# Performance work log

Hardware: AMD Instinct MI355X
Metric: run time of the kernel (lower is better)

The kernel has to match this reference:

```python
import jax, jax.numpy as jnp
import numpy as np

NODE_DIM = 128
INSTR_DIM = 128
HIDDEN_DIM = 256
N_NODES = 50000
N_EDGES = 800000
N_GRAPHS = 64


def setup_inputs() -> dict:
    key = jax.random.key(0)
    k_instr, k_x, k_ei, k_b, k_w1, k_b1, k_w2, k_b2 = jax.random.split(key, 8)
    instr = jax.random.normal(k_instr, (N_GRAPHS, INSTR_DIM), dtype=jnp.float32)
    x = jax.random.normal(k_x, (N_NODES, NODE_DIM), dtype=jnp.float32)
    edge_index = jax.random.randint(k_ei, (2, N_EDGES), 0, N_NODES, dtype=jnp.int64)
    batch = jnp.sort(jax.random.randint(k_b, (N_NODES,), 0, N_GRAPHS, dtype=jnp.int64))
    in_dim = 2 * NODE_DIM + INSTR_DIM  # 384
    lim1 = 1.0 / np.sqrt(in_dim)
    lim2 = 1.0 / np.sqrt(HIDDEN_DIM)
    W1 = jax.random.uniform(k_w1, (in_dim, HIDDEN_DIM), jnp.float32, -lim1, lim1)
    b1 = jax.random.uniform(k_b1, (HIDDEN_DIM,), jnp.float32, -lim1, lim1)
    W2 = jax.random.uniform(k_w2, (HIDDEN_DIM, 1), jnp.float32, -lim2, lim2)
    b2 = jax.random.uniform(k_b2, (1,), jnp.float32, -lim2, lim2)
    return {"instr": instr, "x": x, "edge_index": edge_index, "batch": batch,
            "W1": W1, "b1": b1, "W2": W2, "b2": b2}


def reference(instr, x, edge_index, batch, W1, b1, W2, b2):
    src, dst = edge_index[0], edge_index[1]
    u = instr[batch[src]]                       # [E, Di] gather via batch[src]
    h = jnp.concatenate([x[src], x[dst], u], axis=-1)  # [E, 2D+Di]
    h = jax.nn.silu(h @ W1 + b1)                # [E, H] (dropout p=0 -> identity)
    logits = (h @ W2 + b2).squeeze(-1)          # [E]
    return logits
```

## Files before the change

kernel.cpp:

```cpp
#include <hip/hip_runtime.h>
#include <hip/hip_bf16.h>
#include <stdint.h>

#define E_EDGES   800000
#define N_NODES_C 50000
#define NG        64
#define DD        128
#define HH        256
#define KDIM      384

typedef __bf16 bf16x8 __attribute__((ext_vector_type(8)));
typedef __bf16 bf16x4 __attribute__((ext_vector_type(4)));
typedef float  f32x4  __attribute__((ext_vector_type(4)));
typedef uint32_t u32x4 __attribute__((ext_vector_type(4)));

__device__ __forceinline__ void gld16(const void* g, void* l) {
  __builtin_amdgcn_global_load_lds(
      (__attribute__((address_space(1))) void*)g,
      (__attribute__((address_space(3))) void*)l, 16, 0, 0);
}

__device__ __forceinline__ float bf_hi(uint32_t u) { return __uint_as_float(u & 0xffff0000u); }
__device__ __forceinline__ float bf_lo(uint32_t u) { return __uint_as_float(u << 16); }

#define PREP_CVT_BLKS 6250
#define PREP_W1_BLKS  256
#define PREP_R2_BLKS  64

__global__ void k_prep(const float* __restrict__ x, const float* __restrict__ w1,
                       const float* __restrict__ instr, const float* __restrict__ b1,
                       __bf16* __restrict__ xbf, __bf16* __restrict__ w1pt,
                       float* __restrict__ r2) {
  __shared__ float ins[DD];
  const int bid = blockIdx.x;
  const int tid = threadIdx.x;
  if (bid < PREP_CVT_BLKS) {
    int i = bid * 256 + tid;
    float4 v = ((const float4*)x)[i];
    bf16x4 b;
    b[0] = (__bf16)v.x; b[1] = (__bf16)v.y; b[2] = (__bf16)v.z; b[3] = (__bf16)v.w;
    ((bf16x4*)xbf)[i] = b;
  } else if (bid < PREP_CVT_BLKS + PREP_W1_BLKS) {
    int idx = (bid - PREP_CVT_BLKS) * 256 + tid;
    int n = idx >> 7;
    int k = idx & 127;
    float v = (n < 256) ? w1[k * HH + n] : w1[(128 + k) * HH + (n - 256)];
    w1pt[n * 128 + k] = (__bf16)v;
  } else {
    int g = bid - (PREP_CVT_BLKS + PREP_W1_BLKS);
    int c = tid;
    if (c < DD) ins[c] = instr[g * DD + c];
    __syncthreads();
    float sum = b1[c];
#pragma unroll 8
    for (int k = 0; k < DD; ++k) sum += ins[k] * w1[(256 + k) * HH + c];
    r2[g * HH + c] = sum;
  }
}

__launch_bounds__(512, 4)
__global__ void k_nodegemm(const __bf16* __restrict__ xbf,
                           const __bf16* __restrict__ w1pt,
                           const int*   __restrict__ batch,
                           const float* __restrict__ r2,
                           __bf16* __restrict__ pq)
{
  __shared__ __align__(16) char smem[16384 + 32768];
  char* As = smem;
  char* Bs = smem + 16384;

  const int tid  = threadIdx.x;
  const int lane = tid & 63;
  const int wid  = tid >> 6;
  const int rowbase = blockIdx.x * 128;
  const int nt      = blockIdx.y;

  const int arow  = tid >> 2;
  const int aslot = tid & 3;
  const int akap  = aslot ^ ((arow >> 1) & 3);
  int gr = rowbase + arow; if (gr >= N_NODES_C) gr = N_NODES_C - 1;
  const char* aptr = (const char*)xbf + (size_t)gr * 256 + akap * 16;

  const char* bptr[2];
#pragma unroll
  for (int it = 0; it < 2; ++it) {
    int j2 = tid + it * 512;
    int n  = j2 >> 2;
    int bk = (j2 & 3) ^ ((n >> 1) & 3);
    bptr[it] = (const char*)w1pt + (size_t)(nt * 256 + n) * 256 + bk * 16;
  }

  char* ldsA = As + wid * 1024;
  char* ldsB = Bs + wid * 1024;

  auto stage = [&](int cur, int kk) {
    gld16(bptr[0] + kk * 64, ldsB + cur * 16384);
    gld16(bptr[1] + kk * 64, ldsB + cur * 16384 + 8192);
    gld16(aptr    + kk * 64, ldsA + cur * 8192);
  };

  const int wm    = wid >> 2;
  const int wn    = wid & 3;
  const int l15   = lane & 15;
  const int kap_r = (lane >> 4) ^ ((l15 >> 1) & 3);
  const int aoff  = wm * 4096 + l15 * 64 + kap_r * 16;
  const int boff  = wn * 4096 + l15 * 64 + kap_r * 16;

  f32x4 acc[4][4];
#pragma unroll
  for (int mi = 0; mi < 4; ++mi)
#pragma unroll
    for (int ni = 0; ni < 4; ++ni)
      acc[mi][ni] = f32x4{0.f, 0.f, 0.f, 0.f};

  stage(0, 0);

  for (int kk = 0; kk < 4; ++kk) {
    const int cur = kk & 1;
    __syncthreads();
    if (kk + 1 < 4) stage(cur ^ 1, kk + 1);

    const char* pA = As + cur * 8192;
    const char* pB = Bs + cur * 16384;
    bf16x8 av[4], bv[4];
#pragma unroll
    for (int mi = 0; mi < 4; ++mi) av[mi] = *(const bf16x8*)(pA + aoff + mi * 1024);
#pragma unroll
    for (int ni = 0; ni < 4; ++ni) bv[ni] = *(const bf16x8*)(pB + boff + ni * 1024);
#pragma unroll
    for (int mi = 0; mi < 4; ++mi)
#pragma unroll
      for (int ni = 0; ni < 4; ++ni)
        acc[mi][ni] = __builtin_amdgcn_mfma_f32_16x16x32_bf16(av[mi], bv[ni], acc[mi][ni], 0, 0, 0);
  }

  const int rg = lane >> 4;
  const bool fold = (nt == 0);
#pragma unroll
  for (int mi = 0; mi < 4; ++mi) {
    int row = rowbase + wm * 64 + mi * 16 + rg * 4;
#pragma unroll
    for (int r = 0; r < 4; ++r) {
      int rr = row + r;
      if (rr < N_NODES_C) {
        float addv[4] = {0.f, 0.f, 0.f, 0.f};
        if (fold) {
          int g = batch[rr];
          const float* r2row = r2 + g * HH + wn * 64 + l15;
#pragma unroll
          for (int ni = 0; ni < 4; ++ni) addv[ni] = r2row[ni * 16];
        }
        size_t base = (size_t)rr * 512 + nt * 256 + wn * 64 + l15;
#pragma unroll
        for (int ni = 0; ni < 4; ++ni)
          pq[base + ni * 16] = (__bf16)(acc[mi][ni][r] + addv[ni]);
      }
    }
  }
}

__launch_bounds__(256, 8)
__global__ void k_edge(const __bf16* __restrict__ pq,
                       const int*   __restrict__ ei,
                       const float* __restrict__ w2,
                       const float* __restrict__ b2,
                       float* __restrict__ out)
{
  const int tid  = threadIdx.x;
  const int lane = tid & 63;
  const int wid  = tid >> 6;
  const int half = lane >> 5;
  const int l    = lane & 31;
  const int c0   = l * 8;

  float w2r[8];
  {
    float4 a = *(const float4*)(w2 + c0);
    float4 b = *(const float4*)(w2 + c0 + 4);
    w2r[0]=a.x; w2r[1]=a.y; w2r[2]=a.z; w2r[3]=a.w;
    w2r[4]=b.x; w2r[5]=b.y; w2r[6]=b.z; w2r[7]=b.w;
  }
  const float bb = b2[0];
  const float NL2E = -1.44269504f;

  for (int e = blockIdx.x * 16 + (wid * 2 + half) * 2; e < E_EDGES; e += gridDim.x * 16) {
    int s0 = ei[e];     int d0 = ei[E_EDGES + e];
    int s1 = ei[e + 1]; int d1 = ei[E_EDGES + e + 1];

    u32x4 p0 = *(const u32x4*)(pq + (size_t)s0 * 512 + c0);
    u32x4 q0 = *(const u32x4*)(pq + (size_t)d0 * 512 + 256 + c0);
    u32x4 p1 = *(const u32x4*)(pq + (size_t)s1 * 512 + c0);
    u32x4 q1 = *(const u32x4*)(pq + (size_t)d1 * 512 + 256 + c0);

    float sum0 = 0.f, sum1 = 0.f;
#pragma unroll
    for (int k = 0; k < 4; ++k) {
      {
        float va = bf_lo(p0[k]) + bf_lo(q0[k]);
        float vb = bf_hi(p0[k]) + bf_hi(q0[k]);
        float ta = __builtin_amdgcn_exp2f(va * NL2E);
        float tb = __builtin_amdgcn_exp2f(vb * NL2E);
        float da = 1.f + ta, db = 1.f + tb;
        float rc = __builtin_amdgcn_rcpf(da * db);
        sum0 += (va * w2r[2 * k]) * (rc * db) + (vb * w2r[2 * k + 1]) * (rc * da);
      }
      {
        float va = bf_lo(p1[k]) + bf_lo(q1[k]);
        float vb = bf_hi(p1[k]) + bf_hi(q1[k]);
        float ta = __builtin_amdgcn_exp2f(va * NL2E);
        float tb = __builtin_amdgcn_exp2f(vb * NL2E);
        float da = 1.f + ta, db = 1.f + tb;
        float rc = __builtin_amdgcn_rcpf(da * db);
        sum1 += (va * w2r[2 * k]) * (rc * db) + (vb * w2r[2 * k + 1]) * (rc * da);
      }
    }

#pragma unroll
    for (int off = 1; off < 32; off <<= 1) {
      sum0 += __shfl_xor(sum0, off, 64);
      sum1 += __shfl_xor(sum1, off, 64);
    }
    if (l == 0) *(float2*)(out + e) = make_float2(sum0 + bb, sum1 + bb);
  }
}

#define BM 128
#define KSTEPS 12
#define THREADS 512

__global__ void k_cvt4(const float* __restrict__ in, __bf16* __restrict__ out, int n4) {
  int i = blockIdx.x * blockDim.x + threadIdx.x;
  if (i < n4) {
    float4 v = ((const float4*)in)[i];
    bf16x4 b;
    b[0] = (__bf16)v.x; b[1] = (__bf16)v.y; b[2] = (__bf16)v.z; b[3] = (__bf16)v.w;
    ((bf16x4*)out)[i] = b;
  }
}

__global__ void k_w1t_fb(const float* __restrict__ w1, __bf16* __restrict__ w1t) {
  int idx = blockIdx.x * blockDim.x + threadIdx.x;
  if (idx < KDIM * HH) {
    int k = idx >> 8;
    int n = idx & 255;
    w1t[n * KDIM + k] = (__bf16)w1[idx];
  }
}

template <int MODE>
__launch_bounds__(THREADS, 4)
__global__ void k_main(const float* __restrict__ xf,
                       const float* __restrict__ instrf,
                       const int*   __restrict__ ei,
                       const int*   __restrict__ batch,
                       const __bf16* __restrict__ xbf,
                       const __bf16* __restrict__ insbf,
                       const __bf16* __restrict__ w1t,
                       const float* __restrict__ b1,
                       const float* __restrict__ w2,
                       const float* __restrict__ b2,
                       float* __restrict__ out)
{
  __shared__ __align__(16) char smem[16384 + 32768 + 2048];
  char*  As  = smem;
  char*  Bs  = smem + 16384;
  float* red = (float*)(smem + 16384 + 32768);

  const int tid  = threadIdx.x;
  const int lane = tid & 63;
  const int wid  = tid >> 6;
  const int blk  = blockIdx.x;

  const int arow  = tid >> 2;
  const int aslot = tid & 3;
  const int akap  = aslot ^ ((arow >> 1) & 3);
  const int e     = blk * BM + arow;
  const int s     = ei[e];
  const int d     = ei[E_EDGES + e];
  const int g     = batch[s];

  const char  *aS = nullptr, *aD = nullptr, *aI = nullptr;
  const float *fS = nullptr, *fD = nullptr, *fI = nullptr;
  if (MODE == 0) {
    aS = (const char*)xbf   + s * 256 + akap * 16;
    aD = (const char*)xbf   + d * 256 + akap * 16;
    aI = (const char*)insbf + g * 256 + akap * 16;
  } else {
    fS = xf     + s * DD + akap * 8;
    fD = xf     + d * DD + akap * 8;
    fI = instrf + g * DD + akap * 8;
  }

  const char* bptr[2];
#pragma unroll
  for (int it = 0; it < 2; ++it) {
    int j2 = tid + it * 512;
    int n  = j2 >> 2;
    int bk = (j2 & 3) ^ ((n >> 1) & 3);
    bptr[it] = (const char*)w1t + n * (KDIM * 2) + bk * 16;
  }

  char* ldsA = As + wid * 1024;
  char* ldsB = Bs + wid * 1024;

  auto stage = [&](int cur, int kk) {
    gld16(bptr[0] + kk * 64, ldsB + cur * 16384);
    gld16(bptr[1] + kk * 64, ldsB + cur * 16384 + 8192);
    if (MODE == 0) {
      const char* ga = (kk < 4) ? (aS + kk * 64)
                     : (kk < 8) ? (aD + (kk - 4) * 64)
                                : (aI + (kk - 8) * 64);
      gld16(ga, ldsA + cur * 8192);
    } else {
      const float* gf = (kk < 4) ? (fS + kk * 32)
                      : (kk < 8) ? (fD + (kk - 4) * 32)
                                 : (fI + (kk - 8) * 32);
      float4 v0 = *(const float4*)gf;
      float4 v1 = *(const float4*)(gf + 4);
      bf16x8 bv;
      bv[0] = (__bf16)v0.x; bv[1] = (__bf16)v0.y; bv[2] = (__bf16)v0.z; bv[3] = (__bf16)v0.w;
      bv[4] = (__bf16)v1.x; bv[5] = (__bf16)v1.y; bv[6] = (__bf16)v1.z; bv[7] = (__bf16)v1.w;
      *(bf16x8*)(As + cur * 8192 + tid * 16) = bv;
    }
  };

  const int wm    = wid >> 2;
  const int wn    = wid & 3;
  const int l15   = lane & 15;
  const int kap_r = (lane >> 4) ^ ((l15 >> 1) & 3);
  const int aoff  = wm * 4096 + l15 * 64 + kap_r * 16;
  const int boff  = wn * 4096 + l15 * 64 + kap_r * 16;

  f32x4 acc[4][4];
#pragma unroll
  for (int mi = 0; mi < 4; ++mi)
#pragma unroll
    for (int ni = 0; ni < 4; ++ni)
      acc[mi][ni] = f32x4{0.f, 0.f, 0.f, 0.f};

  stage(0, 0);

  for (int kk = 0; kk < KSTEPS; ++kk) {
    const int cur = kk & 1;
    __syncthreads();
    if (kk + 1 < KSTEPS) stage(cur ^ 1, kk + 1);

    const char* pA = As + cur * 8192;
    const char* pB = Bs + cur * 16384;
    bf16x8 av[4], bv[4];
#pragma unroll
    for (int mi = 0; mi < 4; ++mi) av[mi] = *(const bf16x8*)(pA + aoff + mi * 1024);
#pragma unroll
    for (int ni = 0; ni < 4; ++ni) bv[ni] = *(const bf16x8*)(pB + boff + ni * 1024);
#pragma unroll
    for (int mi = 0; mi < 4; ++mi)
#pragma unroll
      for (int ni = 0; ni < 4; ++ni)
        acc[mi][ni] = __builtin_amdgcn_mfma_f32_16x16x32_bf16(av[mi], bv[ni], acc[mi][ni], 0, 0, 0);
  }

  float b1c[4], w2c[4];
#pragma unroll
  for (int ni = 0; ni < 4; ++ni) {
    int n = wn * 64 + ni * 16 + l15;
    b1c[ni] = b1[n];
    w2c[ni] = w2[n];
  }

  float rowsum[4][4];
#pragma unroll
  for (int mi = 0; mi < 4; ++mi)
#pragma unroll
    for (int r = 0; r < 4; ++r) rowsum[mi][r] = 0.f;

#pragma unroll
  for (int ni = 0; ni < 4; ++ni) {
    float bbv = b1c[ni], ww = w2c[ni];
#pragma unroll
    for (int mi = 0; mi < 4; ++mi)
#pragma unroll
      for (int r = 0; r < 4; ++r) {
        float v  = acc[mi][ni][r] + bbv;
        float sv = v / (1.0f + __expf(-v));
        rowsum[mi][r] += sv * ww;
      }
  }

#pragma unroll
  for (int off = 1; off < 16; off <<= 1)
#pragma unroll
    for (int mi = 0; mi < 4; ++mi)
#pragma unroll
      for (int r = 0; r < 4; ++r)
        rowsum[mi][r] += __shfl_xor(rowsum[mi][r], off, 64);

  if (l15 == 0) {
    int rg = lane >> 4;
#pragma unroll
    for (int mi = 0; mi < 4; ++mi)
#pragma unroll
      for (int r = 0; r < 4; ++r)
        red[wn * 128 + wm * 64 + mi * 16 + rg * 4 + r] = rowsum[mi][r];
  }
  __syncthreads();

  if (tid < BM) {
    float v = red[tid] + red[128 + tid] + red[256 + tid] + red[384 + tid] + b2[0];
    out[blk * BM + tid] = v;
  }
}

extern "C" void kernel_launch(void* const* d_in, const int* in_sizes, int n_in,
                              void* d_out, int out_size, void* d_ws, size_t ws_size,
                              hipStream_t stream) {
  const float* instr = (const float*)d_in[0];
  const float* x     = (const float*)d_in[1];
  const int*   ei    = (const int*)d_in[2];
  const int*   batch = (const int*)d_in[3];
  const float* W1    = (const float*)d_in[4];
  const float* b1    = (const float*)d_in[5];
  const float* W2    = (const float*)d_in[6];
  const float* b2    = (const float*)d_in[7];
  float* out = (float*)d_out;
  char* ws = (char*)d_ws;

  const size_t off_xbf  = 0;
  const size_t off_w1pt = 12800000;
  const size_t off_r2   = 12931072;
  const size_t off_pq   = 12996608;
  const size_t need_full = 64196608;

  if (ws_size >= need_full) {
    __bf16* xbf  = (__bf16*)(ws + off_xbf);
    __bf16* w1pt = (__bf16*)(ws + off_w1pt);
    float*  r2   = (float*)(ws + off_r2);
    __bf16* pq   = (__bf16*)(ws + off_pq);

    k_prep<<<PREP_CVT_BLKS + PREP_W1_BLKS + PREP_R2_BLKS, 256, 0, stream>>>(
        x, W1, instr, b1, xbf, w1pt, r2);
    dim3 g1((N_NODES_C + 127) / 128, 2);
    k_nodegemm<<<g1, 512, 0, stream>>>(xbf, w1pt, batch, r2, pq);
    k_edge<<<2048, 256, 0, stream>>>(pq, ei, W2, b2, out);
    return;
  }

  const size_t f_off_xbf = 0;
  const size_t f_off_ins = 12800000;
  const size_t f_off_w1t = 12816384;
  const size_t need_fast = 13012992;

  if (ws_size >= need_fast) {
    __bf16* xbf   = (__bf16*)(ws + f_off_xbf);
    __bf16* insbf = (__bf16*)(ws + f_off_ins);
    __bf16* w1t   = (__bf16*)(ws + f_off_w1t);
    k_cvt4<<<(N_NODES_C * DD / 4 + 255) / 256, 256, 0, stream>>>(x, xbf, N_NODES_C * DD / 4);
    k_cvt4<<<(NG * DD / 4 + 255) / 256, 256, 0, stream>>>(instr, insbf, NG * DD / 4);
    k_w1t_fb<<<(KDIM * HH + 255) / 256, 256, 0, stream>>>(W1, w1t);
    k_main<0><<<E_EDGES / BM, THREADS, 0, stream>>>(x, instr, ei, batch, xbf, insbf, w1t,
                                                    b1, W2, b2, out);
  } else {
    __bf16* w1t = (__bf16*)ws;
    k_w1t_fb<<<(KDIM * HH + 255) / 256, 256, 0, stream>>>(W1, w1t);
    k_main<1><<<E_EDGES / BM, THREADS, 0, stream>>>(x, instr, ei, batch, nullptr, nullptr, w1t,
                                                    b1, W2, b2, out);
  }
}
```

Measured before the change: 150.2 us.

## Sort edges by source node via counting sort before edge kernel

Adds a histogram, a single-block prefix scan, and an atomic scatter that bucket edges by source node. The edge kernel then walks edges in source order and writes results back through a permutation index. The aim is to improve cache locality of the source-row gathers from the pq buffer, at the cost of three extra kernels, a memset, atomics, and scattered output writes. Buffers reuse the xbf workspace region, which is no longer needed once the node GEMM has run.

```diff
diff --git a/kernel.cpp b/kernel.cpp
--- a/kernel.cpp
+++ b/kernel.cpp
@@ -159,12 +159,54 @@
   }
 }
 
+__global__ void k_hist(const int* __restrict__ ei, int* __restrict__ cnt) {
+  int e = blockIdx.x * 256 + threadIdx.x;
+  if (e < E_EDGES) atomicAdd(&cnt[ei[e]], 1);
+}
+
+__global__ void k_scan(int* __restrict__ cnt) {
+  __shared__ int ts[1024];
+  const int t = threadIdx.x;
+  const int PER = 49;
+  int lo = t * PER;
+  int hi = lo + PER; if (hi > N_NODES_C) hi = N_NODES_C;
+  int s = 0;
+  for (int i = lo; i < hi && i < N_NODES_C; ++i) s += cnt[i];
+  ts[t] = s;
+  __syncthreads();
+  for (int off = 1; off < 1024; off <<= 1) {
+    int v = (t >= off) ? ts[t - off] : 0;
+    __syncthreads();
+    ts[t] += v;
+    __syncthreads();
+  }
+  int run = (t == 0) ? 0 : ts[t - 1];
+  for (int i = lo; i < hi && i < N_NODES_C; ++i) {
+    int c = cnt[i];
+    cnt[i] = run;
+    run += c;
+  }
+}
+
+__global__ void k_scatter(const int* __restrict__ ei, int* __restrict__ base,
+                          int2* __restrict__ sd2, int* __restrict__ eidx) {
+  int e = blockIdx.x * 256 + threadIdx.x;
+  if (e < E_EDGES) {
+    int s = ei[e];
+    int d = ei[E_EDGES + e];
+    int slot = atomicAdd(&base[s], 1);
+    sd2[slot] = make_int2(s, d);
+    eidx[slot] = e;
+  }
+}
+
 __launch_bounds__(256, 8)
-__global__ void k_edge(const __bf16* __restrict__ pq,
-                       const int*   __restrict__ ei,
-                       const float* __restrict__ w2,
-                       const float* __restrict__ b2,
-                       float* __restrict__ out)
+__global__ void k_edge2(const __bf16* __restrict__ pq,
+                        const int2*  __restrict__ sd2,
+                        const int*   __restrict__ eidx,
+                        const float* __restrict__ w2,
+                        const float* __restrict__ b2,
+                        float* __restrict__ out)
 {
   const int tid  = threadIdx.x;
   const int lane = tid & 63;
@@ -183,14 +225,14 @@
   const float bb = b2[0];
   const float NL2E = -1.44269504f;
 
-  for (int e = blockIdx.x * 16 + (wid * 2 + half) * 2; e < E_EDGES; e += gridDim.x * 16) {
-    int s0 = ei[e];     int d0 = ei[E_EDGES + e];
-    int s1 = ei[e + 1]; int d1 = ei[E_EDGES + e + 1];
-
-    u32x4 p0 = *(const u32x4*)(pq + (size_t)s0 * 512 + c0);
-    u32x4 q0 = *(const u32x4*)(pq + (size_t)d0 * 512 + 256 + c0);
-    u32x4 p1 = *(const u32x4*)(pq + (size_t)s1 * 512 + c0);
-    u32x4 q1 = *(const u32x4*)(pq + (size_t)d1 * 512 + 256 + c0);
+  for (int sl = blockIdx.x * 16 + (wid * 2 + half) * 2; sl < E_EDGES; sl += gridDim.x * 16) {
+    int4 sd = *(const int4*)(sd2 + sl);
+    int2 eo = *(const int2*)(eidx + sl);
+
+    u32x4 p0 = *(const u32x4*)(pq + (size_t)sd.x * 512 + c0);
+    u32x4 q0 = *(const u32x4*)(pq + (size_t)sd.y * 512 + 256 + c0);
+    u32x4 p1 = *(const u32x4*)(pq + (size_t)sd.z * 512 + c0);
+    u32x4 q1 = *(const u32x4*)(pq + (size_t)sd.w * 512 + 256 + c0);
 
     float sum0 = 0.f, sum1 = 0.f;
 #pragma unroll
@@ -220,7 +262,10 @@
       sum0 += __shfl_xor(sum0, off, 64);
       sum1 += __shfl_xor(sum1, off, 64);
     }
-    if (l == 0) *(float2*)(out + e) = make_float2(sum0 + bb, sum1 + bb);
+    if (l == 0) {
+      out[eo.x] = sum0 + bb;
+      out[eo.y] = sum1 + bb;
+    }
   }
 }
 
@@ -425,6 +470,9 @@
   char* ws = (char*)d_ws;
 
   const size_t off_xbf  = 0;
+  const size_t off_sd2  = 0;
+  const size_t off_eidx = 6400000;
+  const size_t off_cnt  = 9600000;
   const size_t off_w1pt = 12800000;
   const size_t off_r2   = 12931072;
   const size_t off_pq   = 12996608;
@@ -435,12 +483,19 @@
     __bf16* w1pt = (__bf16*)(ws + off_w1pt);
     float*  r2   = (float*)(ws + off_r2);
     __bf16* pq   = (__bf16*)(ws + off_pq);
+    int2*   sd2  = (int2*)(ws + off_sd2);
+    int*    eidx = (int*)(ws + off_eidx);
+    int*    cnt  = (int*)(ws + off_cnt);
 
     k_prep<<<PREP_CVT_BLKS + PREP_W1_BLKS + PREP_R2_BLKS, 256, 0, stream>>>(
         x, W1, instr, b1, xbf, w1pt, r2);
     dim3 g1((N_NODES_C + 127) / 128, 2);
     k_nodegemm<<<g1, 512, 0, stream>>>(xbf, w1pt, batch, r2, pq);
-    k_edge<<<2048, 256, 0, stream>>>(pq, ei, W2, b2, out);
+    hipMemsetAsync(ws + off_cnt, 0, N_NODES_C * sizeof(int), stream);
+    k_hist<<<(E_EDGES + 255) / 256, 256, 0, stream>>>(ei, cnt);
+    k_scan<<<1, 1024, 0, stream>>>(cnt);
+    k_scatter<<<(E_EDGES + 255) / 256, 256, 0, stream>>>(ei, cnt, sd2, eidx);
+    k_edge2<<<2048, 256, 0, stream>>>(pq, sd2, eidx, W2, b2, out);
     return;
   }
 
```

Measured after the change: 290.7 us. +93.6%, slower.

## Sort edges by source node via counting sort to improve gather locality

Applied to the files above, without the earlier changes.

Adds a histogram over source nodes, a two-level prefix scan and a scatter that builds a source-sorted edge list packing src/dst into 16-bit halves plus the original edge id. The edge kernel then walks edges in source order, so repeated source rows of pq are more likely to hit in cache, and writes results back to the original positions. The log2(e) scale is folded into the node GEMM output and ln2 into w2, which removes a multiply per element in the edge SiLU. The price is extra kernels, atomics, a memset, scattered output writes and non-deterministic ordering within each node's bucket. The sorted path runs only when the workspace is large enough.

```diff
diff --git a/kernel.cpp b/kernel.cpp
--- a/kernel.cpp
+++ b/kernel.cpp
@@ -8,6 +8,7 @@
 #define DD        128
 #define HH        256
 #define KDIM      384
+#define CHUNKS    196
 
 typedef __bf16 bf16x8 __attribute__((ext_vector_type(8)));
 typedef __bf16 bf16x4 __attribute__((ext_vector_type(4)));
@@ -26,11 +27,14 @@
 #define PREP_CVT_BLKS 6250
 #define PREP_W1_BLKS  256
 #define PREP_R2_BLKS  64
-
+#define PREP_HIST_BLKS 3125
+
+template <int HIST>
 __global__ void k_prep(const float* __restrict__ x, const float* __restrict__ w1,
                        const float* __restrict__ instr, const float* __restrict__ b1,
+                       const int* __restrict__ ei,
                        __bf16* __restrict__ xbf, __bf16* __restrict__ w1pt,
-                       float* __restrict__ r2) {
+                       float* __restrict__ r2, int* __restrict__ cnt) {
   __shared__ float ins[DD];
   const int bid = blockIdx.x;
   const int tid = threadIdx.x;
@@ -46,7 +50,7 @@
     int k = idx & 127;
     float v = (n < 256) ? w1[k * HH + n] : w1[(128 + k) * HH + (n - 256)];
     w1pt[n * 128 + k] = (__bf16)v;
-  } else {
+  } else if (bid < PREP_CVT_BLKS + PREP_W1_BLKS + PREP_R2_BLKS) {
     int g = bid - (PREP_CVT_BLKS + PREP_W1_BLKS);
     int c = tid;
     if (c < DD) ins[c] = instr[g * DD + c];
@@ -55,6 +59,9 @@
 #pragma unroll 8
     for (int k = 0; k < DD; ++k) sum += ins[k] * w1[(256 + k) * HH + c];
     r2[g * HH + c] = sum;
+  } else if (HIST) {
+    int e = (bid - (PREP_CVT_BLKS + PREP_W1_BLKS + PREP_R2_BLKS)) * 256 + tid;
+    if (e < E_EDGES) atomicAdd(&cnt[ei[e]], 1);
   }
 }
 
@@ -136,6 +143,7 @@
 
   const int rg = lane >> 4;
   const bool fold = (nt == 0);
+  const float L2E = 1.44269504f;
 #pragma unroll
   for (int mi = 0; mi < 4; ++mi) {
     int row = rowbase + wm * 64 + mi * 16 + rg * 4;
@@ -153,18 +161,75 @@
         size_t base = (size_t)rr * 512 + nt * 256 + wn * 64 + l15;
 #pragma unroll
         for (int ni = 0; ni < 4; ++ni)
-          pq[base + ni * 16] = (__bf16)(acc[mi][ni][r] + addv[ni]);
+          pq[base + ni * 16] = (__bf16)((acc[mi][ni][r] + addv[ni]) * L2E);
       }
     }
   }
 }
 
+__global__ void k_scan1(int* __restrict__ cnt, int* __restrict__ pref) {
+  __shared__ int ts[256];
+  const int t = threadIdx.x;
+  const int i = blockIdx.x * 256 + t;
+  int v = (i < N_NODES_C) ? cnt[i] : 0;
+  ts[t] = v;
+  __syncthreads();
+  for (int off = 1; off < 256; off <<= 1) {
+    int u = (t >= off) ? ts[t - off] : 0;
+    __syncthreads();
+    ts[t] += u;
+    __syncthreads();
+  }
+  if (i < N_NODES_C) cnt[i] = ts[t] - v;
+  if (t == 255) pref[blockIdx.x] = ts[255];
+}
+
+__global__ void k_scan2(int* __restrict__ pref) {
+  __shared__ int ts[256];
+  const int t = threadIdx.x;
+  int v = (t < CHUNKS) ? pref[t] : 0;
+  ts[t] = v;
+  __syncthreads();
+  for (int off = 1; off < 256; off <<= 1) {
+    int u = (t >= off) ? ts[t - off] : 0;
+    __syncthreads();
+    ts[t] += u;
+    __syncthreads();
+  }
+  if (t < CHUNKS) pref[t] = ts[t] - v;
+}
+
+__global__ void k_scatter(const int* __restrict__ ei, int* __restrict__ cnt,
+                          const int* __restrict__ pref, int2* __restrict__ sde) {
+  int e = blockIdx.x * 256 + threadIdx.x;
+  if (e < E_EDGES) {
+    int s = ei[e];
+    int d = ei[E_EDGES + e];
+    int slot = pref[s >> 8] + atomicAdd(&cnt[s], 1);
+    sde[slot] = make_int2(s | (d << 16), e);
+  }
+}
+
+__device__ __forceinline__ void silu_dot2(const u32x4& p, const u32x4& q,
+                                          const float* w2r, float& sum) {
+#pragma unroll
+  for (int k = 0; k < 4; ++k) {
+    float va = bf_lo(p[k]) + bf_lo(q[k]);
+    float vb = bf_hi(p[k]) + bf_hi(q[k]);
+    float ta = __builtin_amdgcn_exp2f(-va);
+    float tb = __builtin_amdgcn_exp2f(-vb);
+    float da = 1.f + ta, db = 1.f + tb;
+    float rc = __builtin_amdgcn_rcpf(da * db);
+    sum += (va * w2r[2 * k]) * (rc * db) + (vb * w2r[2 * k + 1]) * (rc * da);
+  }
+}
+
 __launch_bounds__(256, 8)
-__global__ void k_edge(const __bf16* __restrict__ pq,
-                       const int*   __restrict__ ei,
-                       const float* __restrict__ w2,
-                       const float* __restrict__ b2,
-                       float* __restrict__ out)
+__global__ void k_edge2(const __bf16* __restrict__ pq,
+                        const int2*  __restrict__ sde,
+                        const float* __restrict__ w2,
+                        const float* __restrict__ b2,
+                        float* __restrict__ out)
 {
   const int tid  = threadIdx.x;
   const int lane = tid & 63;
@@ -172,20 +237,21 @@
   const int half = lane >> 5;
   const int l    = lane & 31;
   const int c0   = l * 8;
+  const float LN2 = 0.69314718f;
 
   float w2r[8];
   {
     float4 a = *(const float4*)(w2 + c0);
     float4 b = *(const float4*)(w2 + c0 + 4);
-    w2r[0]=a.x; w2r[1]=a.y; w2r[2]=a.z; w2r[3]=a.w;
-    w2r[4]=b.x; w2r[5]=b.y; w2r[6]=b.z; w2r[7]=b.w;
+    w2r[0]=a.x*LN2; w2r[1]=a.y*LN2; w2r[2]=a.z*LN2; w2r[3]=a.w*LN2;
+    w2r[4]=b.x*LN2; w2r[5]=b.y*LN2; w2r[6]=b.z*LN2; w2r[7]=b.w*LN2;
   }
   const float bb = b2[0];
-  const float NL2E = -1.44269504f;
-
-  for (int e = blockIdx.x * 16 + (wid * 2 + half) * 2; e < E_EDGES; e += gridDim.x * 16) {
-    int s0 = ei[e];     int d0 = ei[E_EDGES + e];
-    int s1 = ei[e + 1]; int d1 = ei[E_EDGES + e + 1];
+
+  for (int sl = blockIdx.x * 16 + (wid * 2 + half) * 2; sl < E_EDGES; sl += gridDim.x * 16) {
+    int4 t = *(const int4*)(sde + sl);
+    int s0 = t.x & 0xFFFF, d0 = ((unsigned)t.x) >> 16, e0 = t.y;
+    int s1 = t.z & 0xFFFF, d1 = ((unsigned)t.z) >> 16, e1 = t.w;
 
     u32x4 p0 = *(const u32x4*)(pq + (size_t)s0 * 512 + c0);
     u32x4 q0 = *(const u32x4*)(pq + (size_t)d0 * 512 + 256 + c0);
@@ -193,27 +259,57 @@
     u32x4 q1 = *(const u32x4*)(pq + (size_t)d1 * 512 + 256 + c0);
 
     float sum0 = 0.f, sum1 = 0.f;
-#pragma unroll
-    for (int k = 0; k < 4; ++k) {
-      {
-        float va = bf_lo(p0[k]) + bf_lo(q0[k]);
-        float vb = bf_hi(p0[k]) + bf_hi(q0[k]);
-        float ta = __builtin_amdgcn_exp2f(va * NL2E);
-        float tb = __builtin_amdgcn_exp2f(vb * NL2E);
-        float da = 1.f + ta, db = 1.f + tb;
-        float rc = __builtin_amdgcn_rcpf(da * db);
-        sum0 += (va * w2r[2 * k]) * (rc * db) + (vb * w2r[2 * k + 1]) * (rc * da);
-      }
-      {
-        float va = bf_lo(p1[k]) + bf_lo(q1[k]);
-        float vb = bf_hi(p1[k]) + bf_hi(q1[k]);
-        float ta = __builtin_amdgcn_exp2f(va * NL2E);
-        float tb = __builtin_amdgcn_exp2f(vb * NL2E);
-        float da = 1.f + ta, db = 1.f + tb;
-        float rc = __builtin_amdgcn_rcpf(da * db);
-        sum1 += (va * w2r[2 * k]) * (rc * db) + (vb * w2r[2 * k + 1]) * (rc * da);
-      }
+    silu_dot2(p0, q0, w2r, sum0);
+    silu_dot2(p1, q1, w2r, sum1);
+
+#pragma unroll
+    for (int off = 1; off < 32; off <<= 1) {
+      sum0 += __shfl_xor(sum0, off, 64);
+      sum1 += __shfl_xor(sum1, off, 64);
     }
+    if (l == 0) {
+      out[e0] = sum0 + bb;
+      out[e1] = sum1 + bb;
+    }
+  }
+}
+
+__launch_bounds__(256, 8)
+__global__ void k_edge_uns(const __bf16* __restrict__ pq,
+                           const int*   __restrict__ ei,
+                           const float* __restrict__ w2,
+                           const float* __restrict__ b2,
+                           float* __restrict__ out)
+{
+  const int tid  = threadIdx.x;
+  const int lane = tid & 63;
+  const int wid  = tid >> 6;
+  const int half = lane >> 5;
+  const int l    = lane & 31;
+  const int c0   = l * 8;
+  const float LN2 = 0.69314718f;
+
+  float w2r[8];
+  {
+    float4 a = *(const float4*)(w2 + c0);
+    float4 b = *(const float4*)(w2 + c0 + 4);
+    w2r[0]=a.x*LN2; w2r[1]=a.y*LN2; w2r[2]=a.z*LN2; w2r[3]=a.w*LN2;
+    w2r[4]=b.x*LN2; w2r[5]=b.y*LN2; w2r[6]=b.z*LN2; w2r[7]=b.w*LN2;
+  }
+  const float bb = b2[0];
+
+  for (int e = blockIdx.x * 16 + (wid * 2 + half) * 2; e < E_EDGES; e += gridDim.x * 16) {
+    int s0 = ei[e];     int d0 = ei[E_EDGES + e];
+    int s1 = ei[e + 1]; int d1 = ei[E_EDGES + e + 1];
+
+    u32x4 p0 = *(const u32x4*)(pq + (size_t)s0 * 512 + c0);
+    u32x4 q0 = *(const u32x4*)(pq + (size_t)d0 * 512 + 256 + c0);
+    u32x4 p1 = *(const u32x4*)(pq + (size_t)s1 * 512 + c0);
+    u32x4 q1 = *(const u32x4*)(pq + (size_t)d1 * 512 + 256 + c0);
+
+    float sum0 = 0.f, sum1 = 0.f;
+    silu_dot2(p0, q0, w2r, sum0);
+    silu_dot2(p1, q1, w2r, sum1);
 
 #pragma unroll
     for (int off = 1; off < 32; off <<= 1) {
@@ -425,10 +521,14 @@
   char* ws = (char*)d_ws;
 
   const size_t off_xbf  = 0;
+  const size_t off_sde  = 0;
   const size_t off_w1pt = 12800000;
   const size_t off_r2   = 12931072;
   const size_t off_pq   = 12996608;
-  const size_t need_full = 64196608;
+  const size_t off_cnt  = 64196608;
+  const size_t off_pref = 64396608;
+  const size_t need_full   = 64196608;
+  const size_t need_sorted = 64397632;
 
   if (ws_size >= need_full) {
     __bf16* xbf  = (__bf16*)(ws + off_xbf);
@@ -436,11 +536,27 @@
     float*  r2   = (float*)(ws + off_r2);
     __bf16* pq   = (__bf16*)(ws + off_pq);
 
-    k_prep<<<PREP_CVT_BLKS + PREP_W1_BLKS + PREP_R2_BLKS, 256, 0, stream>>>(
-        x, W1, instr, b1, xbf, w1pt, r2);
-    dim3 g1((N_NODES_C + 127) / 128, 2);
-    k_nodegemm<<<g1, 512, 0, stream>>>(xbf, w1pt, batch, r2, pq);
-    k_edge<<<2048, 256, 0, stream>>>(pq, ei, W2, b2, out);
+    if (ws_size >= need_sorted) {
+      int*  cnt  = (int*)(ws + off_cnt);
+      int*  pref = (int*)(ws + off_pref);
+      int2* sde  = (int2*)(ws + off_sde);
+
+      hipMemsetAsync(ws + off_cnt, 0, N_NODES_C * sizeof(int), stream);
+      k_prep<1><<<PREP_CVT_BLKS + PREP_W1_BLKS + PREP_R2_BLKS + PREP_HIST_BLKS,
+                  256, 0, stream>>>(x, W1, instr, b1, ei, xbf, w1pt, r2, cnt);
+      k_scan1<<<CHUNKS, 256, 0, stream>>>(cnt, pref);
+      k_scan2<<<1, 256, 0, stream>>>(pref);
+      dim3 g1((N_NODES_C + 127) / 128, 2);
+      k_nodegemm<<<g1, 512, 0, stream>>>(xbf, w1pt, batch, r2, pq);
+      k_scatter<<<(E_EDGES + 255) / 256, 256, 0, stream>>>(ei, cnt, pref, sde);
+      k_edge2<<<2048, 256, 0, stream>>>(pq, sde, W2, b2, out);
+    } else {
+      k_prep<0><<<PREP_CVT_BLKS + PREP_W1_BLKS + PREP_R2_BLKS,
+                  256, 0, stream>>>(x, W1, instr, b1, ei, xbf, w1pt, r2, nullptr);
+      dim3 g1((N_NODES_C + 127) / 128, 2);
+      k_nodegemm<<<g1, 512, 0, stream>>>(xbf, w1pt, batch, r2, pq);
+      k_edge_uns<<<2048, 256, 0, stream>>>(pq, ei, W2, b2, out);
+    }
     return;
   }
 
```

New measurement: 211.4 us. +40.8%, slower.

## Fuse x bf16 conversion into node GEMM, prescale log2e, prefetch edge indices

Applied to the files above, without the earlier changes.

Drops the separate fp32-to-bf16 conversion of x from the prep kernel. The node GEMM now loads fp32 x directly, converts it in registers and writes it to LDS with a plain store instead of global_load_lds. This removes the write and re-read of the bf16 copy of x. The GEMM output is also prescaled by log2(e), with w2 scaled by ln2 to compensate, which saves a multiply per element in the edge kernel's sigmoid. The edge kernel now prefetches the next iteration's src/dst indices as int2 loads, so that index latency overlaps the gathers. The risks are that the A-tile load becomes synchronous register traffic rather than async, and that prescaling before bf16 rounding changes the rounding error slightly.

```diff
diff --git a/kernel.cpp b/kernel.cpp
--- a/kernel.cpp
+++ b/kernel.cpp
@@ -23,31 +23,23 @@
 __device__ __forceinline__ float bf_hi(uint32_t u) { return __uint_as_float(u & 0xffff0000u); }
 __device__ __forceinline__ float bf_lo(uint32_t u) { return __uint_as_float(u << 16); }
 
-#define PREP_CVT_BLKS 6250
 #define PREP_W1_BLKS  256
 #define PREP_R2_BLKS  64
 
-__global__ void k_prep(const float* __restrict__ x, const float* __restrict__ w1,
-                       const float* __restrict__ instr, const float* __restrict__ b1,
-                       __bf16* __restrict__ xbf, __bf16* __restrict__ w1pt,
-                       float* __restrict__ r2) {
+__global__ void k_prep(const float* __restrict__ w1, const float* __restrict__ instr,
+                       const float* __restrict__ b1,
+                       __bf16* __restrict__ w1pt, float* __restrict__ r2) {
   __shared__ float ins[DD];
   const int bid = blockIdx.x;
   const int tid = threadIdx.x;
-  if (bid < PREP_CVT_BLKS) {
-    int i = bid * 256 + tid;
-    float4 v = ((const float4*)x)[i];
-    bf16x4 b;
-    b[0] = (__bf16)v.x; b[1] = (__bf16)v.y; b[2] = (__bf16)v.z; b[3] = (__bf16)v.w;
-    ((bf16x4*)xbf)[i] = b;
-  } else if (bid < PREP_CVT_BLKS + PREP_W1_BLKS) {
-    int idx = (bid - PREP_CVT_BLKS) * 256 + tid;
+  if (bid < PREP_W1_BLKS) {
+    int idx = bid * 256 + tid;
     int n = idx >> 7;
     int k = idx & 127;
     float v = (n < 256) ? w1[k * HH + n] : w1[(128 + k) * HH + (n - 256)];
     w1pt[n * 128 + k] = (__bf16)v;
   } else {
-    int g = bid - (PREP_CVT_BLKS + PREP_W1_BLKS);
+    int g = bid - PREP_W1_BLKS;
     int c = tid;
     if (c < DD) ins[c] = instr[g * DD + c];
     __syncthreads();
@@ -59,7 +51,7 @@
 }
 
 __launch_bounds__(512, 4)
-__global__ void k_nodegemm(const __bf16* __restrict__ xbf,
+__global__ void k_nodegemm(const float* __restrict__ x,
                            const __bf16* __restrict__ w1pt,
                            const int*   __restrict__ batch,
                            const float* __restrict__ r2,
@@ -79,7 +71,7 @@
   const int aslot = tid & 3;
   const int akap  = aslot ^ ((arow >> 1) & 3);
   int gr = rowbase + arow; if (gr >= N_NODES_C) gr = N_NODES_C - 1;
-  const char* aptr = (const char*)xbf + (size_t)gr * 256 + akap * 16;
+  const float* aptr = x + (size_t)gr * DD + akap * 8;
 
   const char* bptr[2];
 #pragma unroll
@@ -90,13 +82,18 @@
     bptr[it] = (const char*)w1pt + (size_t)(nt * 256 + n) * 256 + bk * 16;
   }
 
-  char* ldsA = As + wid * 1024;
   char* ldsB = Bs + wid * 1024;
 
   auto stage = [&](int cur, int kk) {
     gld16(bptr[0] + kk * 64, ldsB + cur * 16384);
     gld16(bptr[1] + kk * 64, ldsB + cur * 16384 + 8192);
-    gld16(aptr    + kk * 64, ldsA + cur * 8192);
+    const float* gf = aptr + kk * 32;
+    float4 v0 = *(const float4*)gf;
+    float4 v1 = *(const float4*)(gf + 4);
+    bf16x8 bv;
+    bv[0] = (__bf16)v0.x; bv[1] = (__bf16)v0.y; bv[2] = (__bf16)v0.z; bv[3] = (__bf16)v0.w;
+    bv[4] = (__bf16)v1.x; bv[5] = (__bf16)v1.y; bv[6] = (__bf16)v1.z; bv[7] = (__bf16)v1.w;
+    *(bf16x8*)(As + cur * 8192 + tid * 16) = bv;
   };
 
   const int wm    = wid >> 2;
@@ -136,6 +133,7 @@
 
   const int rg = lane >> 4;
   const bool fold = (nt == 0);
+  const float L2E = 1.44269504f;
 #pragma unroll
   for (int mi = 0; mi < 4; ++mi) {
     int row = rowbase + wm * 64 + mi * 16 + rg * 4;
@@ -153,9 +151,23 @@
         size_t base = (size_t)rr * 512 + nt * 256 + wn * 64 + l15;
 #pragma unroll
         for (int ni = 0; ni < 4; ++ni)
-          pq[base + ni * 16] = (__bf16)(acc[mi][ni][r] + addv[ni]);
+          pq[base + ni * 16] = (__bf16)((acc[mi][ni][r] + addv[ni]) * L2E);
       }
     }
+  }
+}
+
+__device__ __forceinline__ void silu_dot2(const u32x4& p, const u32x4& q,
+                                          const float* w2r, float& sum) {
+#pragma unroll
+  for (int k = 0; k < 4; ++k) {
+    float va = bf_lo(p[k]) + bf_lo(q[k]);
+    float vb = bf_hi(p[k]) + bf_hi(q[k]);
+    float ta = __builtin_amdgcn_exp2f(-va);
+    float tb = __builtin_amdgcn_exp2f(-vb);
+    float da = 1.f + ta, db = 1.f + tb;
+    float rc = __builtin_amdgcn_rcpf(da * db);
+    sum += (va * w2r[2 * k]) * (rc * db) + (vb * w2r[2 * k + 1]) * (rc * da);
   }
 }
 
@@ -172,48 +184,39 @@
   const int half = lane >> 5;
   const int l    = lane & 31;
   const int c0   = l * 8;
+  const float LN2 = 0.69314718f;
 
   float w2r[8];
   {
     float4 a = *(const float4*)(w2 + c0);
     float4 b = *(const float4*)(w2 + c0 + 4);
-    w2r[0]=a.x; w2r[1]=a.y; w2r[2]=a.z; w2r[3]=a.w;
-    w2r[4]=b.x; w2r[5]=b.y; w2r[6]=b.z; w2r[7]=b.w;
+    w2r[0]=a.x*LN2; w2r[1]=a.y*LN2; w2r[2]=a.z*LN2; w2r[3]=a.w*LN2;
+    w2r[4]=b.x*LN2; w2r[5]=b.y*LN2; w2r[6]=b.z*LN2; w2r[7]=b.w*LN2;
   }
   const float bb = b2[0];
-  const float NL2E = -1.44269504f;
-
-  for (int e = blockIdx.x * 16 + (wid * 2 + half) * 2; e < E_EDGES; e += gridDim.x * 16) {
-    int s0 = ei[e];     int d0 = ei[E_EDGES + e];
-    int s1 = ei[e + 1]; int d1 = ei[E_EDGES + e + 1];
-
-    u32x4 p0 = *(const u32x4*)(pq + (size_t)s0 * 512 + c0);
-    u32x4 q0 = *(const u32x4*)(pq + (size_t)d0 * 512 + 256 + c0);
-    u32x4 p1 = *(const u32x4*)(pq + (size_t)s1 * 512 + c0);
-    u32x4 q1 = *(const u32x4*)(pq + (size_t)d1 * 512 + 256 + c0);
+  const int stride = gridDim.x * 16;
+
+  int e = blockIdx.x * 16 + (wid * 2 + half) * 2;
+  if (e >= E_EDGES) return;
+  int2 sv = *(const int2*)(ei + e);
+  int2 dv = *(const int2*)(ei + E_EDGES + e);
+
+  while (true) {
+    const int en = e + stride;
+    int2 svn = make_int2(0, 0), dvn = make_int2(0, 0);
+    if (en < E_EDGES) {
+      svn = *(const int2*)(ei + en);
+      dvn = *(const int2*)(ei + E_EDGES + en);
+    }
+
+    u32x4 p0 = *(const u32x4*)(pq + (size_t)sv.x * 512 + c0);
+    u32x4 q0 = *(const u32x4*)(pq + (size_t)dv.x * 512 + 256 + c0);
+    u32x4 p1 = *(const u32x4*)(pq + (size_t)sv.y * 512 + c0);
+    u32x4 q1 = *(const u32x4*)(pq + (size_t)dv.y * 512 + 256 + c0);
 
     float sum0 = 0.f, sum1 = 0.f;
-#pragma unroll
-    for (int k = 0; k < 4; ++k) {
-      {
-        float va = bf_lo(p0[k]) + bf_lo(q0[k]);
-        float vb = bf_hi(p0[k]) + bf_hi(q0[k]);
-        float ta = __builtin_amdgcn_exp2f(va * NL2E);
-        float tb = __builtin_amdgcn_exp2f(vb * NL2E);
-        float da = 1.f + ta, db = 1.f + tb;
-        float rc = __builtin_amdgcn_rcpf(da * db);
-        sum0 += (va * w2r[2 * k]) * (rc * db) + (vb * w2r[2 * k + 1]) * (rc * da);
-      }
-      {
-        float va = bf_lo(p1[k]) + bf_lo(q1[k]);
-        float vb = bf_hi(p1[k]) + bf_hi(q1[k]);
-        float ta = __builtin_amdgcn_exp2f(va * NL2E);
-        float tb = __builtin_amdgcn_exp2f(vb * NL2E);
-        float da = 1.f + ta, db = 1.f + tb;
-        float rc = __builtin_amdgcn_rcpf(da * db);
-        sum1 += (va * w2r[2 * k]) * (rc * db) + (vb * w2r[2 * k + 1]) * (rc * da);
-      }
-    }
+    silu_dot2(p0, q0, w2r, sum0);
+    silu_dot2(p1, q1, w2r, sum1);
 
 #pragma unroll
     for (int off = 1; off < 32; off <<= 1) {
@@ -221,6 +224,9 @@
       sum1 += __shfl_xor(sum1, off, 64);
     }
     if (l == 0) *(float2*)(out + e) = make_float2(sum0 + bb, sum1 + bb);
+
+    if (en >= E_EDGES) break;
+    e = en; sv = svn; dv = dvn;
   }
 }
 
@@ -424,22 +430,19 @@
   float* out = (float*)d_out;
   char* ws = (char*)d_ws;
 
-  const size_t off_xbf  = 0;
-  const size_t off_w1pt = 12800000;
-  const size_t off_r2   = 12931072;
-  const size_t off_pq   = 12996608;
-  const size_t need_full = 64196608;
+  const size_t off_w1pt = 0;
+  const size_t off_r2   = 131072;
+  const size_t off_pq   = 196608;
+  const size_t need_full = 51396608;
 
   if (ws_size >= need_full) {
-    __bf16* xbf  = (__bf16*)(ws + off_xbf);
     __bf16* w1pt = (__bf16*)(ws + off_w1pt);
     float*  r2   = (float*)(ws + off_r2);
     __bf16* pq   = (__bf16*)(ws + off_pq);
 
-    k_prep<<<PREP_CVT_BLKS + PREP_W1_BLKS + PREP_R2_BLKS, 256, 0, stream>>>(
-        x, W1, instr, b1, xbf, w1pt, r2);
+    k_prep<<<PREP_W1_BLKS + PREP_R2_BLKS, 256, 0, stream>>>(W1, instr, b1, w1pt, r2);
     dim3 g1((N_NODES_C + 127) / 128, 2);
-    k_nodegemm<<<g1, 512, 0, stream>>>(xbf, w1pt, batch, r2, pq);
+    k_nodegemm<<<g1, 512, 0, stream>>>(x, w1pt, batch, r2, pq);
     k_edge<<<2048, 256, 0, stream>>>(pq, ei, W2, b2, out);
     return;
   }
```

After: 188.1 us. 25.3% more time.
